# Kernel tuning notes

Hardware: AMD Instinct MI355X
Metric: run time of the kernel (lower is better)

The kernel has to match this reference:

```python
import jax, jax.numpy as jnp
import numpy as np

B, N, T, F, NC = 4, 16, 2048, 512, 43
EPS = 1e-5


def setup_inputs() -> dict:
    key = jax.random.key(0)
    ks = jax.random.split(key, 8)
    bbox = jax.random.normal(ks[0], (B, N, 4, T), jnp.float32)
    bbox_class = jax.random.randint(ks[1], (B, N, T), 0, NC, jnp.int32)
    edge_map = jax.random.uniform(ks[2], (B, N, N, T), jnp.float32)
    W_lin = jax.random.normal(ks[3], (F, 4), jnp.float32) * 0.1          # nn.Linear(4, F) weight [F,4]
    emb_table = jax.random.normal(ks[4], (NC, F), jnp.float32) * 0.1
    emb_table = emb_table.at[0].set(0.0)                                  # padding_idx=0
    W1 = jax.random.normal(ks[5], (F, 2 * F), jnp.float32) * (1.0 / np.sqrt(2 * F))  # 1x1 conv2d [F,2F]
    W2 = jax.random.normal(ks[6], (F, F), jnp.float32) * (1.0 / np.sqrt(F))          # 1x1 conv2d [F,F]
    Wm = jax.random.normal(ks[7], (F, F, N), jnp.float32) * (1.0 / np.sqrt(F * N))   # conv1d merge [F,F,N]
    ln_w = jnp.ones((F,), jnp.float32)
    ln_b = jnp.zeros((F,), jnp.float32)
    return {"bbox": bbox, "bbox_class": bbox_class, "edge_map": edge_map,
            "W_lin": W_lin, "emb_table": emb_table, "W1": W1, "W2": W2,
            "Wm": Wm, "ln_w": ln_w, "ln_b": ln_b}


def reference(bbox, bbox_class, edge_map, W_lin, emb_table, W1, W2, Wm, ln_w, ln_b):
    # edge_map [B,N,N,T] -> [B,T,N,N]
    em = jnp.transpose(edge_map, (0, 3, 1, 2))
    # class embedding: [B,N,T] -> [B,T,N] -> [B,T,N,F]
    cls_e = emb_table[jnp.transpose(bbox_class, (0, 2, 1))]
    # bbox linear: [B,N,4,T] x [F,4] -> [B,T,N,F]
    box_e = jnp.einsum('bnct,fc->btnf', bbox, W_lin)
    # cat along features: note original concatenates (class_embed, bbox_embed)
    node = jnp.concatenate([cls_e, box_e], axis=-1)        # [B,T,N,2F]
    node = jnp.einsum('btnc,fc->btnf', node, W1)           # 1x1 conv
    node = jax.nn.relu(jnp.einsum('btij,btjf->btif', em, node))
    node = jnp.einsum('btnc,fc->btnf', node, W2)           # 1x1 conv
    node = jax.nn.relu(jnp.einsum('btij,btjf->btif', em, node))
    # conv1d over node axis with kernel size N collapses N: [B,T,F]
    feat = jnp.einsum('btnc,fcn->btf', node, Wm)
    # LayerNorm over channel dim of [B,F,T]
    x = jnp.transpose(feat, (0, 2, 1))                     # [B,F,T]
    mu = jnp.mean(x, axis=1, keepdims=True)
    r = x - mu
    var = jnp.mean(r * r, axis=1, keepdims=True)
    out = r / jnp.sqrt(var + EPS)
    return out * ln_w[None, :, None] + ln_b[None, :, None]
```

## Files before the change

kernel.cpp:

```cpp
#include <hip/hip_runtime.h>
#include <hip/hip_bf16.h>

#define B_  4
#define N_  16
#define T_  2048
#define F_  512
#define NC_ 43
constexpr float LN_EPS = 1e-5f;

constexpr int EMB1_N = NC_ * F_;
constexpr int WBOX_N = F_ * 4;
constexpr int W2BF_N = F_ * F_;
constexpr int WMT_N  = F_ * N_ * F_;
constexpr int K_TOT  = N_ * F_;
constexpr long long GBUF_N = (long long)B_ * T_ * N_ * F_;

typedef __bf16 bf16x8_t __attribute__((ext_vector_type(8)));
typedef float  f32x4_t  __attribute__((ext_vector_type(4)));

__device__ __forceinline__ void gload16(const void* g, void* l) {
  __builtin_amdgcn_global_load_lds(
      (const __attribute__((address_space(1))) unsigned int*)g,
      (__attribute__((address_space(3))) unsigned int*)l, 16, 0, 0);
}

__device__ __forceinline__ short bf16s(float x) {
  return (short)__bfloat16_as_ushort(__float2bfloat16(x));
}
__device__ __forceinline__ unsigned bf16u(float x) {
  return (unsigned)__bfloat16_as_ushort(__float2bfloat16(x));
}

__global__ __launch_bounds__(256) void precompute_small(
    const float* __restrict__ emb_table, const float* __restrict__ W1,
    const float* __restrict__ W_lin, const float* __restrict__ W2,
    float* __restrict__ emb1, float* __restrict__ wbox,
    __hip_bfloat16* __restrict__ w2bf)
{
  int idx = blockIdx.x * 256 + threadIdx.x;
  if (idx < EMB1_N) {
    int k = idx >> 9, f = idx & 511;
    const float4* et = (const float4*)&emb_table[k * F_];
    const float4* w1 = (const float4*)&W1[f * (2 * F_)];
    float s = 0.f;
    for (int c4 = 0; c4 < F_ / 4; ++c4) {
      float4 a = et[c4], b = w1[c4];
      s = fmaf(a.x, b.x, s); s = fmaf(a.y, b.y, s);
      s = fmaf(a.z, b.z, s); s = fmaf(a.w, b.w, s);
    }
    emb1[idx] = s;
  } else if (idx < EMB1_N + WBOX_N) {
    int t2 = idx - EMB1_N;
    int f = t2 >> 2, q = t2 & 3;
    const float4* w1 = (const float4*)&W1[f * (2 * F_) + F_];
    float s = 0.f;
    for (int c4 = 0; c4 < F_ / 4; ++c4) {
      float4 a = w1[c4];
      s = fmaf(a.x, W_lin[(c4 * 4 + 0) * 4 + q], s);
      s = fmaf(a.y, W_lin[(c4 * 4 + 1) * 4 + q], s);
      s = fmaf(a.z, W_lin[(c4 * 4 + 2) * 4 + q], s);
      s = fmaf(a.w, W_lin[(c4 * 4 + 3) * 4 + q], s);
    }
    wbox[t2] = s;
  } else if (idx < EMB1_N + WBOX_N + W2BF_N) {
    int t3 = idx - (EMB1_N + WBOX_N);
    w2bf[t3] = __float2bfloat16(W2[t3]);
  }
}

__global__ __launch_bounds__(256) void precompute_wmT(
    const float* __restrict__ Wm, __hip_bfloat16* __restrict__ wmT)
{
  __shared__ float tile[16 * 517];
  const int f = blockIdx.x;
  const float* src = Wm + (long long)f * 8192;
  for (int i = threadIdx.x; i < 8192; i += 256) {
    int c = i >> 4, n = i & 15;
    tile[n * 517 + c] = src[i];
  }
  __syncthreads();
  short* dst = (short*)wmT + (long long)f * 8192;
  for (int i = threadIdx.x; i < 4096; i += 256) {
    int o = i << 1;
    int n = o >> 9, c = o & 511;
    short2 sv;
    sv.x = bf16s(tile[n * 517 + c]);
    sv.y = bf16s(tile[n * 517 + c + 1]);
    *(short2*)&dst[o] = sv;
  }
}

#define N1ST 20
__global__ __launch_bounds__(256) void k_h1g(
    const float* __restrict__ bbox, const int* __restrict__ cls,
    const float* __restrict__ edge, const float* __restrict__ emb1,
    const float* __restrict__ wbox, __hip_bfloat16* __restrict__ g,
    int pbase)
{
  __shared__ __align__(16) short em_bf[256];
  __shared__ __align__(16) short n1T[F_ * N1ST + 32];
  __shared__ int   cls_s[N_];
  __shared__ float bb_s[N_ * 4];

  const int p = blockIdx.x;
  const int pg = p + pbase;
  const int b = pg >> 11;
  const int t = pg & 2047;
  const int tid = threadIdx.x;

  {
    int i = tid >> 4, j = tid & 15;
    em_bf[tid] = bf16s(edge[(((b * N_ + i) * N_ + j) * T_) + t]);
  }
  if (tid < N_) cls_s[tid] = cls[(b * N_ + tid) * T_ + t];
  if (tid < N_ * 4) {
    int j = tid >> 2, qq = tid & 3;
    bb_s[tid] = bbox[(((b * N_ + j) * 4 + qq) * T_) + t];
  }
  __syncthreads();

  const float4* wb4 = (const float4*)wbox;
  for (int idx = tid; idx < N_ * F_ / 4; idx += 256) {
    int j = idx >> 7, f4 = idx & 127;
    float4 e = *(const float4*)&emb1[cls_s[j] * F_ + f4 * 4];
    float b0 = bb_s[j * 4 + 0], b1 = bb_s[j * 4 + 1];
    float b2 = bb_s[j * 4 + 2], b3 = bb_s[j * 4 + 3];
    float4 w0 = wb4[f4 * 4 + 0], w1 = wb4[f4 * 4 + 1];
    float4 w2 = wb4[f4 * 4 + 2], w3 = wb4[f4 * 4 + 3];
    int f = f4 * 4;
    float v0 = e.x; v0 = fmaf(b0, w0.x, v0); v0 = fmaf(b1, w0.y, v0);
    v0 = fmaf(b2, w0.z, v0); v0 = fmaf(b3, w0.w, v0);
    float v1 = e.y; v1 = fmaf(b0, w1.x, v1); v1 = fmaf(b1, w1.y, v1);
    v1 = fmaf(b2, w1.z, v1); v1 = fmaf(b3, w1.w, v1);
    float v2 = e.z; v2 = fmaf(b0, w2.x, v2); v2 = fmaf(b1, w2.y, v2);
    v2 = fmaf(b2, w2.z, v2); v2 = fmaf(b3, w2.w, v2);
    float v3 = e.w; v3 = fmaf(b0, w3.x, v3); v3 = fmaf(b1, w3.y, v3);
    v3 = fmaf(b2, w3.z, v3); v3 = fmaf(b3, w3.w, v3);
    n1T[(f + 0) * N1ST + j] = bf16s(v0);
    n1T[(f + 1) * N1ST + j] = bf16s(v1);
    n1T[(f + 2) * N1ST + j] = bf16s(v2);
    n1T[(f + 3) * N1ST + j] = bf16s(v3);
  }
  __syncthreads();

  const int lane = tid & 63, wv = tid >> 6;
  const int c = lane & 15;
  const int q = lane >> 4;

  union { bf16x8_t v; short4 s[2]; } ef;
  ef.s[0] = (short4){0, 0, 0, 0};
  ef.s[1] = (short4){0, 0, 0, 0};
  if (q < 2) {
    ef.s[0] = *(const short4*)&em_bf[c * 16 + 8 * q];
    ef.s[1] = *(const short4*)&em_bf[c * 16 + 8 * q + 4];
  }
  const int ko = (q < 2) ? 8 * q : 0;
  const int a0 = ((32 * q + c) & 63) * 4;
  const int a1 = ((32 * q + 16 + c) & 63) * 4;

  short* gs = (short*)g;
  const long long gbase = (long long)p * (N_ * F_);

#pragma unroll
  for (int tl = 0; tl < 8; ++tl) {
    const int ft = wv * 8 + tl;
    const int row = (ft * 16 + c) * N1ST;

    union { bf16x8_t v; short4 s[2]; } bf_;
    bf_.s[0] = *(const short4*)&n1T[row + ko];
    bf_.s[1] = *(const short4*)&n1T[row + ko + 4];
    f32x4_t d1 = __builtin_amdgcn_mfma_f32_16x16x32_bf16(
        ef.v, bf_.v, (f32x4_t){0.f, 0.f, 0.f, 0.f}, 0, 0, 0);

    int pk0 = (int)((bf16u(fmaxf(d1[1], 0.f)) << 16) | bf16u(fmaxf(d1[0], 0.f)));
    int pk1 = (int)((bf16u(fmaxf(d1[3], 0.f)) << 16) | bf16u(fmaxf(d1[2], 0.f)));

    union { bf16x8_t v; int u[4]; } af_;
    af_.u[0] = __builtin_amdgcn_ds_bpermute(a0, pk0);
    af_.u[1] = __builtin_amdgcn_ds_bpermute(a0, pk1);
    af_.u[2] = __builtin_amdgcn_ds_bpermute(a1, pk0);
    af_.u[3] = __builtin_amdgcn_ds_bpermute(a1, pk1);

    f32x4_t d2 = __builtin_amdgcn_mfma_f32_16x16x32_bf16(
        af_.v, ef.v, (f32x4_t){0.f, 0.f, 0.f, 0.f}, 0, 0, 0);
    short4 gv;
    gv.x = bf16s(d2[0]);
    gv.y = bf16s(d2[1]);
    gv.z = bf16s(d2[2]);
    gv.w = bf16s(d2[3]);
    *(short4*)&gs[gbase + c * F_ + ft * 16 + 4 * q] = gv;
  }
}

__device__ __forceinline__ void stage_d3(const short* gs, const short* ws,
                                         long long m0, int n0, int kc,
                                         short* As, short* Bs,
                                         int rowU, int chkU) {
  gload16(gs + (m0 + rowU) * F_ + kc + chkU, As + rowU * 32 + chkU);
#pragma unroll
  for (int it = 0; it < 2; ++it)
    gload16(ws + (n0 + it * 128 + rowU) * F_ + kc + chkU,
            Bs + (it * 128 + rowU) * 32 + chkU);
}

__global__ __launch_bounds__(512, 2) void gemm_h2_d3(
    const __hip_bfloat16* __restrict__ gIn,
    const __hip_bfloat16* __restrict__ w2bf,
    __hip_bfloat16* __restrict__ h2out)
{
  __shared__ __align__(16) short As[3][128 * 32];
  __shared__ __align__(16) short Bs[3][256 * 32];

  const short* gs = (const short*)gIn;
  const short* ws = (const short*)w2bf;
  short* hs = (short*)h2out;

  const int tid = threadIdx.x;
  const int bx = blockIdx.x;
  const int mt = (bx & 7) | ((bx >> 4) << 3);
  const int nt = (bx >> 3) & 1;
  const long long m0 = (long long)mt * 128;
  const int n0 = nt * 256;

  const int wave8 = tid >> 6, lane = tid & 63;
  const int wr = wave8 >> 2, wcol = wave8 & 3;
  const int rowU = tid >> 2, chkU = (tid & 3) * 8;
  const int mrow = lane & 15, kq = (lane >> 4) * 8;

  f32x4_t acc[4][4];
#pragma unroll
  for (int i = 0; i < 4; ++i)
#pragma unroll
    for (int j = 0; j < 4; ++j) acc[i][j] = (f32x4_t){0.f, 0.f, 0.f, 0.f};

  auto compute = [&](const short* Ap, const short* Bp) {
    bf16x8_t af[4], bfr[4];
#pragma unroll
    for (int i = 0; i < 4; ++i)
      af[i] = *(const bf16x8_t*)&Ap[((wr << 6) + i * 16 + mrow) * 32 + kq];
#pragma unroll
    for (int j = 0; j < 4; ++j)
      bfr[j] = *(const bf16x8_t*)&Bp[((wcol << 6) + j * 16 + mrow) * 32 + kq];
    __builtin_amdgcn_s_setprio(1);
#pragma unroll
    for (int i = 0; i < 4; ++i)
#pragma unroll
      for (int j = 0; j < 4; ++j)
        acc[i][j] = __builtin_amdgcn_mfma_f32_16x16x32_bf16(af[i], bfr[j], acc[i][j], 0, 0, 0);
    __builtin_amdgcn_s_setprio(0);
  };

  stage_d3(gs, ws, m0, n0, 0,  As[0], Bs[0], rowU, chkU);
  stage_d3(gs, ws, m0, n0, 32, As[1], Bs[1], rowU, chkU);
  stage_d3(gs, ws, m0, n0, 64, As[2], Bs[2], rowU, chkU);

  for (int t = 0; t < 13; ++t) {
    asm volatile("s_waitcnt vmcnt(6)" ::: "memory");
    __builtin_amdgcn_sched_barrier(0);
    __builtin_amdgcn_s_barrier();
    __builtin_amdgcn_sched_barrier(0);

    const int s = t % 3;
    compute(As[s], Bs[s]);

    __builtin_amdgcn_sched_barrier(0);
    __builtin_amdgcn_s_barrier();
    __builtin_amdgcn_sched_barrier(0);
    stage_d3(gs, ws, m0, n0, (t + 3) * 32, As[s], Bs[s], rowU, chkU);
  }
  asm volatile("s_waitcnt vmcnt(6)" ::: "memory");
  __builtin_amdgcn_sched_barrier(0);
  __builtin_amdgcn_s_barrier();
  __builtin_amdgcn_sched_barrier(0);
  compute(As[1], Bs[1]);
  asm volatile("s_waitcnt vmcnt(3)" ::: "memory");
  __builtin_amdgcn_sched_barrier(0);
  __builtin_amdgcn_s_barrier();
  __builtin_amdgcn_sched_barrier(0);
  compute(As[2], Bs[2]);
  asm volatile("s_waitcnt vmcnt(0)" ::: "memory");
  __builtin_amdgcn_sched_barrier(0);
  __builtin_amdgcn_s_barrier();
  __builtin_amdgcn_sched_barrier(0);
  compute(As[0], Bs[0]);

  const int rbase = (lane >> 4) << 2;
#pragma unroll
  for (int i = 0; i < 4; ++i)
#pragma unroll
    for (int j = 0; j < 4; ++j)
#pragma unroll
      for (int r = 0; r < 4; ++r) {
        int row = (wr << 6) + i * 16 + rbase + r;
        int col = n0 + (wcol << 6) + j * 16 + mrow;
        float v = fmaxf(acc[i][j][r], 0.f);
        hs[(m0 + row) * F_ + col] = bf16s(v);
      }
}

__device__ __forceinline__ void stage_ip(const short* gs, const short* ws,
                                         long long m0, int kc,
                                         short* As, short* Bs,
                                         int rowU, int chkU) {
  gload16(gs + (m0 + rowU) * F_ + kc + chkU, As + rowU * 32 + chkU);
#pragma unroll
  for (int it = 0; it < 4; ++it)
    gload16(ws + (it * 128 + rowU) * F_ + kc + chkU,
            Bs + (it * 128 + rowU) * 32 + chkU);
}

__global__ __launch_bounds__(512, 2) void gemm_h2_ip(
    __hip_bfloat16* __restrict__ gbuf, const __hip_bfloat16* __restrict__ w2bf)
{
  __shared__ __align__(16) short As[2][128 * 32];
  __shared__ __align__(16) short Bs[2][512 * 32];

  short* gs = (short*)gbuf;
  const short* ws = (const short*)w2bf;

  const int tid = threadIdx.x;
  const long long m0 = (long long)blockIdx.x * 128;
  const int wave8 = tid >> 6, lane = tid & 63;
  const int wr = wave8 >> 2, wcol = wave8 & 3;
  const int rowU = tid >> 2, chkU = (tid & 3) * 8;
  const int mrow = lane & 15, kq = (lane >> 4) * 8;

  f32x4_t acc[4][8];
#pragma unroll
  for (int i = 0; i < 4; ++i)
#pragma unroll
    for (int j = 0; j < 8; ++j) acc[i][j] = (f32x4_t){0.f, 0.f, 0.f, 0.f};

  auto compute = [&](const short* Ap, const short* Bp) {
    bf16x8_t af[4], bfr[8];
#pragma unroll
    for (int i = 0; i < 4; ++i)
      af[i] = *(const bf16x8_t*)&Ap[((wr << 6) + i * 16 + mrow) * 32 + kq];
#pragma unroll
    for (int j = 0; j < 8; ++j)
      bfr[j] = *(const bf16x8_t*)&Bp[((wcol << 7) + j * 16 + mrow) * 32 + kq];
    __builtin_amdgcn_s_setprio(1);
#pragma unroll
    for (int i = 0; i < 4; ++i)
#pragma unroll
      for (int j = 0; j < 8; ++j)
        acc[i][j] = __builtin_amdgcn_mfma_f32_16x16x32_bf16(af[i], bfr[j], acc[i][j], 0, 0, 0);
    __builtin_amdgcn_s_setprio(0);
  };

  stage_ip(gs, ws, m0, 0,  As[0], Bs[0], rowU, chkU);
  stage_ip(gs, ws, m0, 32, As[1], Bs[1], rowU, chkU);

  for (int t = 0; t < 14; ++t) {
    asm volatile("s_waitcnt vmcnt(5)" ::: "memory");
    __builtin_amdgcn_sched_barrier(0);
    __builtin_amdgcn_s_barrier();
    __builtin_amdgcn_sched_barrier(0);

    compute(As[t & 1], Bs[t & 1]);

    __builtin_amdgcn_sched_barrier(0);
    __builtin_amdgcn_s_barrier();
    __builtin_amdgcn_sched_barrier(0);
    stage_ip(gs, ws, m0, (t + 2) * 32, As[t & 1], Bs[t & 1], rowU, chkU);
  }
  asm volatile("s_waitcnt vmcnt(5)" ::: "memory");
  __builtin_amdgcn_sched_barrier(0);
  __builtin_amdgcn_s_barrier();
  __builtin_amdgcn_sched_barrier(0);
  compute(As[0], Bs[0]);
  asm volatile("s_waitcnt vmcnt(0)" ::: "memory");
  __builtin_amdgcn_sched_barrier(0);
  __builtin_amdgcn_s_barrier();
  __builtin_amdgcn_sched_barrier(0);
  compute(As[1], Bs[1]);

  const int rbase = (lane >> 4) << 2;
#pragma unroll
  for (int i = 0; i < 4; ++i)
#pragma unroll
    for (int j = 0; j < 8; ++j)
#pragma unroll
      for (int r = 0; r < 4; ++r) {
        int row = (wr << 6) + i * 16 + rbase + r;
        int col = (wcol << 7) + j * 16 + mrow;
        float v = fmaxf(acc[i][j][r], 0.f);
        gs[(m0 + row) * F_ + col] = bf16s(v);
      }
}

__global__ __launch_bounds__(512, 2) void gemm_feat(
    const __hip_bfloat16* __restrict__ h2g, const __hip_bfloat16* __restrict__ wmTg,
    float* __restrict__ out)
{
  __shared__ __align__(16) char smem[49152];
  float* sM = (float*)smem;
  float* sT = (float*)smem;

  const short* h2s  = (const short*)h2g;
  const short* wmTs = (const short*)wmTg;

  const int tid = threadIdx.x;
  const int bx = blockIdx.x;
  const int mt = bx & 127, nt = bx >> 7;
  const long long m0 = (long long)mt * 64;
  const int n0 = nt * 128;

  const int wave8 = tid >> 6;
  const int half = wave8 >> 2;
  const int wave = wave8 & 3;
  const int lane = tid & 63;
  const int wr = wave >> 1, wc = wave & 1;
  const int mrow = lane & 15;
  const int kq = (lane >> 4) * 8;

  const short* aBase = h2s + m0 * K_TOT;
  const short* bBase = wmTs + (long long)n0 * K_TOT;

  const int rowB = tid >> 2, chkB = (tid & 3) * 8;
  const int hA = tid >> 8;
  const int rA = (tid & 255) >> 2;
  const int kA = (tid & 3) * 8;

  f32x4_t acc[2][4];
#pragma unroll
  for (int i = 0; i < 2; ++i)
#pragma unroll
    for (int j = 0; j < 4; ++j) acc[i][j] = (f32x4_t){0.f, 0.f, 0.f, 0.f};

  for (int ks = 0; ks < 4096; ks += 64) {
#pragma unroll
    for (int s = 0; s < 2; ++s)
      gload16(aBase + (long long)rA * K_TOT + hA * 4096 + ks + s * 32 + kA,
              (short*)(smem + hA * 8192 + s * 4096) + rA * 32 + kA);
#pragma unroll
    for (int h = 0; h < 2; ++h)
#pragma unroll
      for (int s = 0; s < 2; ++s)
        gload16(bBase + (long long)rowB * K_TOT + h * 4096 + ks + s * 32 + chkB,
                (short*)(smem + 16384 + (h * 2 + s) * 8192) + rowB * 32 + chkB);
    __syncthreads();

#pragma unroll
    for (int s = 0; s < 2; ++s) {
      const short* AsH = (const short*)(smem + half * 8192 + s * 4096);
      const short* BsH = (const short*)(smem + 16384 + (half * 2 + s) * 8192);
      bf16x8_t af[2], bfr[4];
#pragma unroll
      for (int i = 0; i < 2; ++i)
        af[i] = *(const bf16x8_t*)&AsH[((wr << 5) + i * 16 + mrow) * 32 + kq];
#pragma unroll
      for (int j = 0; j < 4; ++j)
        bfr[j] = *(const bf16x8_t*)&BsH[((wc << 6) + j * 16 + mrow) * 32 + kq];
#pragma unroll
      for (int i = 0; i < 2; ++i)
#pragma unroll
        for (int j = 0; j < 4; ++j)
          acc[i][j] = __builtin_amdgcn_mfma_f32_16x16x32_bf16(af[i], bfr[j], acc[i][j], 0, 0, 0);
    }
    __syncthreads();
  }

  const int rq = (lane >> 4) << 2;
#pragma unroll
  for (int r = 0; r < 2; ++r) {
    if (half == 1 && wr == r) {
#pragma unroll
      for (int i = 0; i < 2; ++i)
#pragma unroll
        for (int j = 0; j < 4; ++j)
#pragma unroll
          for (int rr = 0; rr < 4; ++rr)
            sM[(i * 16 + rq + rr) * 132 + (wc << 6) + j * 16 + mrow] = acc[i][j][rr];
    }
    __syncthreads();
    if (half == 0 && wr == r) {
#pragma unroll
      for (int i = 0; i < 2; ++i)
#pragma unroll
        for (int j = 0; j < 4; ++j)
#pragma unroll
          for (int rr = 0; rr < 4; ++rr)
            acc[i][j][rr] += sM[(i * 16 + rq + rr) * 132 + (wc << 6) + j * 16 + mrow];
    }
    __syncthreads();
  }

  const int b = (int)(m0 >> 11);
  const int t0 = (int)(m0 & 2047);
#pragma unroll
  for (int cch = 0; cch < 2; ++cch) {
    if (half == 0 && wc == cch) {
#pragma unroll
      for (int i = 0; i < 2; ++i)
#pragma unroll
        for (int j = 0; j < 4; ++j)
#pragma unroll
          for (int rr = 0; rr < 4; ++rr)
            sT[((wr << 5) + i * 16 + rq + rr) * 65 + j * 16 + mrow] = acc[i][j][rr];
    }
    __syncthreads();
    long long ob = (long long)b * (F_ * T_) + (long long)(n0 + cch * 64) * T_ + t0;
    for (int idx = tid; idx < 64 * 64; idx += 512) {
      int f = idx >> 6, m = idx & 63;
      out[ob + (long long)f * T_ + m] = sT[m * 65 + f];
    }
    __syncthreads();
  }
}

__global__ __launch_bounds__(256) void ln_inplace(
    float* __restrict__ out, const float* __restrict__ lnw, const float* __restrict__ lnb)
{
  __shared__ float sF[F_ * 17];
  __shared__ float red[512];
  __shared__ float smu[16], srstd[16];

  const int tid = threadIdx.x;
  const int p0 = blockIdx.x << 4;
  const int b = p0 >> 11, t0 = p0 & 2047;
  long long ob = (long long)b * (F_ * T_) + t0;

  for (int idx = tid; idx < F_ * 16; idx += 256) {
    int f = idx >> 4, m = idx & 15;
    sF[f * 17 + m] = out[ob + (long long)f * T_ + m];
  }
  __syncthreads();

  {
    int m = tid & 15, s = tid >> 4;
    float sum = 0.f, sq = 0.f;
    for (int f = s; f < F_; f += 16) {
      float v = sF[f * 17 + m];
      sum += v; sq += v * v;
    }
    red[tid] = sum;
    red[256 + tid] = sq;
  }
  __syncthreads();
  if (tid < 16) {
    float sum = 0.f, sq = 0.f;
#pragma unroll
    for (int s = 0; s < 16; ++s) { sum += red[s * 16 + tid]; sq += red[256 + s * 16 + tid]; }
    float mu = sum * (1.f / F_);
    float var = sq * (1.f / F_) - mu * mu;
    smu[tid] = mu;
    srstd[tid] = rsqrtf(var + LN_EPS);
  }
  __syncthreads();

  for (int idx = tid; idx < F_ * 16; idx += 256) {
    int f = idx >> 4, m = idx & 15;
    float v = (sF[f * 17 + m] - smu[m]) * srstd[m] * lnw[f] + lnb[f];
    out[ob + (long long)f * T_ + m] = v;
  }
}

extern "C" void kernel_launch(void* const* d_in, const int* in_sizes, int n_in,
                              void* d_out, int out_size, void* d_ws, size_t ws_size,
                              hipStream_t stream)
{
  const float* bbox      = (const float*)d_in[0];
  const int*   cls       = (const int*)d_in[1];
  const float* edge      = (const float*)d_in[2];
  const float* W_lin     = (const float*)d_in[3];
  const float* emb_table = (const float*)d_in[4];
  const float* W1        = (const float*)d_in[5];
  const float* W2        = (const float*)d_in[6];
  const float* Wm        = (const float*)d_in[7];
  const float* lnw       = (const float*)d_in[8];
  const float* lnb       = (const float*)d_in[9];
  float* out = (float*)d_out;

  float* emb1 = (float*)d_ws;
  float* wbox = emb1 + EMB1_N;
  __hip_bfloat16* w2bf = (__hip_bfloat16*)(wbox + WBOX_N);
  __hip_bfloat16* wmT  = w2bf + W2BF_N;
  __hip_bfloat16* wsBase = wmT + WMT_N;

  const size_t base_bytes =
      (size_t)(EMB1_N + WBOX_N) * 4 + (size_t)(W2BF_N + WMT_N) * 2;
  const size_t tier1 = base_bytes + 2ULL * (size_t)GBUF_N * 2;
  const size_t tier2 = base_bytes + (size_t)GBUF_N + (size_t)GBUF_N * 2;

  precompute_small<<<(EMB1_N + WBOX_N + W2BF_N) / 256, 256, 0, stream>>>(
      emb_table, W1, W_lin, W2, emb1, wbox, w2bf);
  precompute_wmT<<<F_, 256, 0, stream>>>(Wm, wmT);

  if (ws_size >= tier1) {
    __hip_bfloat16* gbuf  = wsBase;
    __hip_bfloat16* h2buf = gbuf + GBUF_N;
    k_h1g<<<B_ * T_, 256, 0, stream>>>(bbox, cls, edge, emb1, wbox, gbuf, 0);
    gemm_h2_d3<<<2048, 512, 0, stream>>>(gbuf, w2bf, h2buf);
    gemm_feat<<<512, 512, 0, stream>>>(h2buf, wmT, out);
  } else if (ws_size >= tier2) {
    __hip_bfloat16* gHalf = wsBase;
    __hip_bfloat16* h2buf = gHalf + GBUF_N / 2;
    for (int c = 0; c < 2; ++c) {
      k_h1g<<<B_ * T_ / 2, 256, 0, stream>>>(
          bbox, cls, edge, emb1, wbox, gHalf, c * (B_ * T_ / 2));
      gemm_h2_d3<<<1024, 512, 0, stream>>>(
          gHalf, w2bf, h2buf + (long long)c * (GBUF_N / 2));
    }
    gemm_feat<<<512, 512, 0, stream>>>(h2buf, wmT, out);
  } else {
    __hip_bfloat16* gbuf = wsBase;
    k_h1g<<<B_ * T_, 256, 0, stream>>>(bbox, cls, edge, emb1, wbox, gbuf, 0);
    gemm_h2_ip<<<1024, 512, 0, stream>>>(gbuf, w2bf);
    gemm_feat<<<512, 512, 0, stream>>>(gbuf, wmT, out);
  }
  ln_inplace<<<B_ * T_ / 16, 256, 0, stream>>>(out, lnw, lnb);
}
```

Baseline: 412.3 us.

## Triple-buffer gemm_feat K-loop with async LDS loads and vmcnt-based waits

```diff
diff --git a/kernel.cpp b/kernel.cpp
--- a/kernel.cpp
+++ b/kernel.cpp
@@ -389,11 +389,23 @@
       }
 }
 
+__device__ __forceinline__ void stage_feat(const short* aBase, const short* bBase,
+                                           char* bufBase, int u,
+                                           int hA, int rA, int kA,
+                                           int rowB, int chkB) {
+  gload16(aBase + (long long)rA * K_TOT + hA * 4096 + u * 32 + kA,
+          (short*)(bufBase + hA * 4096) + rA * 32 + kA);
+#pragma unroll
+  for (int h = 0; h < 2; ++h)
+    gload16(bBase + (long long)rowB * K_TOT + h * 4096 + u * 32 + chkB,
+            (short*)(bufBase + 8192 + h * 8192) + rowB * 32 + chkB);
+}
+
 __global__ __launch_bounds__(512, 2) void gemm_feat(
     const __hip_bfloat16* __restrict__ h2g, const __hip_bfloat16* __restrict__ wmTg,
     float* __restrict__ out)
 {
-  __shared__ __align__(16) char smem[49152];
+  __shared__ __align__(16) char smem[73728];
   float* sM = (float*)smem;
   float* sT = (float*)smem;
 
@@ -428,38 +440,62 @@
 #pragma unroll
     for (int j = 0; j < 4; ++j) acc[i][j] = (f32x4_t){0.f, 0.f, 0.f, 0.f};
 
-  for (int ks = 0; ks < 4096; ks += 64) {
-#pragma unroll
-    for (int s = 0; s < 2; ++s)
-      gload16(aBase + (long long)rA * K_TOT + hA * 4096 + ks + s * 32 + kA,
-              (short*)(smem + hA * 8192 + s * 4096) + rA * 32 + kA);
-#pragma unroll
-    for (int h = 0; h < 2; ++h)
-#pragma unroll
-      for (int s = 0; s < 2; ++s)
-        gload16(bBase + (long long)rowB * K_TOT + h * 4096 + ks + s * 32 + chkB,
-                (short*)(smem + 16384 + (h * 2 + s) * 8192) + rowB * 32 + chkB);
-    __syncthreads();
-
-#pragma unroll
-    for (int s = 0; s < 2; ++s) {
-      const short* AsH = (const short*)(smem + half * 8192 + s * 4096);
-      const short* BsH = (const short*)(smem + 16384 + (half * 2 + s) * 8192);
-      bf16x8_t af[2], bfr[4];
-#pragma unroll
-      for (int i = 0; i < 2; ++i)
-        af[i] = *(const bf16x8_t*)&AsH[((wr << 5) + i * 16 + mrow) * 32 + kq];
+  auto computeU = [&](char* bufBase) {
+    const short* AsH = (const short*)(bufBase + half * 4096);
+    const short* BsH = (const short*)(bufBase + 8192 + half * 8192);
+    bf16x8_t af[2], bfr[4];
+#pragma unroll
+    for (int i = 0; i < 2; ++i)
+      af[i] = *(const bf16x8_t*)&AsH[((wr << 5) + i * 16 + mrow) * 32 + kq];
+#pragma unroll
+    for (int j = 0; j < 4; ++j)
+      bfr[j] = *(const bf16x8_t*)&BsH[((wc << 6) + j * 16 + mrow) * 32 + kq];
+    __builtin_amdgcn_s_setprio(1);
+#pragma unroll
+    for (int i = 0; i < 2; ++i)
 #pragma unroll
       for (int j = 0; j < 4; ++j)
-        bfr[j] = *(const bf16x8_t*)&BsH[((wc << 6) + j * 16 + mrow) * 32 + kq];
-#pragma unroll
-      for (int i = 0; i < 2; ++i)
-#pragma unroll
-        for (int j = 0; j < 4; ++j)
-          acc[i][j] = __builtin_amdgcn_mfma_f32_16x16x32_bf16(af[i], bfr[j], acc[i][j], 0, 0, 0);
-    }
-    __syncthreads();
-  }
+        acc[i][j] = __builtin_amdgcn_mfma_f32_16x16x32_bf16(af[i], bfr[j], acc[i][j], 0, 0, 0);
+    __builtin_amdgcn_s_setprio(0);
+  };
+
+  stage_feat(aBase, bBase, smem + 0 * 24576, 0, hA, rA, kA, rowB, chkB);
+  stage_feat(aBase, bBase, smem + 1 * 24576, 1, hA, rA, kA, rowB, chkB);
+  stage_feat(aBase, bBase, smem + 2 * 24576, 2, hA, rA, kA, rowB, chkB);
+
+  for (int u = 0; u < 125; ++u) {
+    asm volatile("s_waitcnt vmcnt(6)" ::: "memory");
+    __builtin_amdgcn_sched_barrier(0);
+    __builtin_amdgcn_s_barrier();
+    __builtin_amdgcn_sched_barrier(0);
+
+    char* buf = smem + (u % 3) * 24576;
+    computeU(buf);
+
+    __builtin_amdgcn_sched_barrier(0);
+    __builtin_amdgcn_s_barrier();
+    __builtin_amdgcn_sched_barrier(0);
+    stage_feat(aBase, bBase, buf, u + 3, hA, rA, kA, rowB, chkB);
+  }
+  asm volatile("s_waitcnt vmcnt(6)" ::: "memory");
+  __builtin_amdgcn_sched_barrier(0);
+  __builtin_amdgcn_s_barrier();
+  __builtin_amdgcn_sched_barrier(0);
+  computeU(smem + (125 % 3) * 24576);
+  asm volatile("s_waitcnt vmcnt(3)" ::: "memory");
+  __builtin_amdgcn_sched_barrier(0);
+  __builtin_amdgcn_s_barrier();
+  __builtin_amdgcn_sched_barrier(0);
+  computeU(smem + (126 % 3) * 24576);
+  asm volatile("s_waitcnt vmcnt(0)" ::: "memory");
+  __builtin_amdgcn_sched_barrier(0);
+  __builtin_amdgcn_s_barrier();
+  __builtin_amdgcn_sched_barrier(0);
+  computeU(smem + (127 % 3) * 24576);
+
+  __builtin_amdgcn_sched_barrier(0);
+  __builtin_amdgcn_s_barrier();
+  __builtin_amdgcn_sched_barrier(0);
 
   const int rq = (lane >> 4) << 2;
 #pragma unroll
```

Measured after the change: 431.2 us. 4.6% more time.

## Double-buffer B tiles in gemm_feat and prefetch loads ahead of MFMA compute

Applied to the files above, without the earlier changes.

```diff
diff --git a/kernel.cpp b/kernel.cpp
--- a/kernel.cpp
+++ b/kernel.cpp
@@ -393,7 +393,7 @@
     const __hip_bfloat16* __restrict__ h2g, const __hip_bfloat16* __restrict__ wmTg,
     float* __restrict__ out)
 {
-  __shared__ __align__(16) char smem[49152];
+  __shared__ __align__(16) char smem[81920];
   float* sM = (float*)smem;
   float* sT = (float*)smem;
 
@@ -428,23 +428,27 @@
 #pragma unroll
     for (int j = 0; j < 4; ++j) acc[i][j] = (f32x4_t){0.f, 0.f, 0.f, 0.f};
 
-  for (int ks = 0; ks < 4096; ks += 64) {
+  auto stageA = [&](int p) {
 #pragma unroll
     for (int s = 0; s < 2; ++s)
-      gload16(aBase + (long long)rA * K_TOT + hA * 4096 + ks + s * 32 + kA,
+      gload16(aBase + (long long)rA * K_TOT + hA * 4096 + p * 64 + s * 32 + kA,
               (short*)(smem + hA * 8192 + s * 4096) + rA * 32 + kA);
+  };
+  auto stageB = [&](int p) {
+    char* bb = smem + 16384 + (p & 1) * 32768;
 #pragma unroll
     for (int h = 0; h < 2; ++h)
 #pragma unroll
       for (int s = 0; s < 2; ++s)
-        gload16(bBase + (long long)rowB * K_TOT + h * 4096 + ks + s * 32 + chkB,
-                (short*)(smem + 16384 + (h * 2 + s) * 8192) + rowB * 32 + chkB);
-    __syncthreads();
-
+        gload16(bBase + (long long)rowB * K_TOT + h * 4096 + p * 64 + s * 32 + chkB,
+                (short*)(bb + (h * 2 + s) * 8192) + rowB * 32 + chkB);
+  };
+  auto computeP = [&](int p) {
+    char* bb = smem + 16384 + (p & 1) * 32768;
 #pragma unroll
     for (int s = 0; s < 2; ++s) {
       const short* AsH = (const short*)(smem + half * 8192 + s * 4096);
-      const short* BsH = (const short*)(smem + 16384 + (half * 2 + s) * 8192);
+      const short* BsH = (const short*)(bb + (half * 2 + s) * 8192);
       bf16x8_t af[2], bfr[4];
 #pragma unroll
       for (int i = 0; i < 2; ++i)
@@ -452,14 +456,55 @@
 #pragma unroll
       for (int j = 0; j < 4; ++j)
         bfr[j] = *(const bf16x8_t*)&BsH[((wc << 6) + j * 16 + mrow) * 32 + kq];
+      __builtin_amdgcn_s_setprio(1);
 #pragma unroll
       for (int i = 0; i < 2; ++i)
 #pragma unroll
         for (int j = 0; j < 4; ++j)
           acc[i][j] = __builtin_amdgcn_mfma_f32_16x16x32_bf16(af[i], bfr[j], acc[i][j], 0, 0, 0);
-    }
-    __syncthreads();
-  }
+      __builtin_amdgcn_s_setprio(0);
+    }
+  };
+
+  stageB(0);
+  __builtin_amdgcn_sched_barrier(0);
+  stageA(0);
+  __builtin_amdgcn_sched_barrier(0);
+  stageB(1);
+
+  for (int p = 0; p < 62; ++p) {
+    asm volatile("s_waitcnt vmcnt(4)" ::: "memory");
+    __builtin_amdgcn_sched_barrier(0);
+    __builtin_amdgcn_s_barrier();
+    __builtin_amdgcn_sched_barrier(0);
+
+    computeP(p);
+
+    __builtin_amdgcn_sched_barrier(0);
+    __builtin_amdgcn_s_barrier();
+    __builtin_amdgcn_sched_barrier(0);
+    stageA(p + 1);
+    __builtin_amdgcn_sched_barrier(0);
+    stageB(p + 2);
+  }
+  asm volatile("s_waitcnt vmcnt(4)" ::: "memory");
+  __builtin_amdgcn_sched_barrier(0);
+  __builtin_amdgcn_s_barrier();
+  __builtin_amdgcn_sched_barrier(0);
+  computeP(62);
+  __builtin_amdgcn_sched_barrier(0);
+  __builtin_amdgcn_s_barrier();
+  __builtin_amdgcn_sched_barrier(0);
+  stageA(63);
+  asm volatile("s_waitcnt vmcnt(0)" ::: "memory");
+  __builtin_amdgcn_sched_barrier(0);
+  __builtin_amdgcn_s_barrier();
+  __builtin_amdgcn_sched_barrier(0);
+  computeP(63);
+
+  __builtin_amdgcn_sched_barrier(0);
+  __builtin_amdgcn_s_barrier();
+  __builtin_amdgcn_sched_barrier(0);
 
   const int rq = (lane >> 4) << 2;
 #pragma unroll
```

After: 401.7 us (median of 2 runs). 1.03x faster.
